# Performance work log

Measured on AMD Instinct MI355X. Metric: run time of the kernel, lower is better.

The kernel has to match this reference:

```python
import jax, jax.numpy as jnp
import numpy as np

N_NODES = 100000
N_EDGES = 1600000
IN_FEATS = 128
OUT_FEATS = 128


def setup_inputs() -> dict:
    key = jax.random.key(0)
    k1, k2, k3, k4, k5 = jax.random.split(key, 5)
    feat = jax.random.normal(k1, (N_NODES, IN_FEATS), dtype=jnp.float32)
    # He (kaiming) uniform-ish init scale for the weights
    bound = np.sqrt(6.0 / IN_FEATS).astype(np.float32)
    weight_u = jax.random.uniform(k2, (IN_FEATS, OUT_FEATS), jnp.float32, -bound, bound)
    weight_v = jax.random.uniform(k3, (IN_FEATS, OUT_FEATS), jnp.float32, -bound, bound)
    bias = jnp.zeros((OUT_FEATS,), dtype=jnp.float32)
    src = jax.random.randint(k4, (N_EDGES,), 0, N_NODES, dtype=jnp.int32)
    dst = jax.random.randint(k5, (N_EDGES,), 0, N_NODES, dtype=jnp.int32)
    return {"feat": feat, "weight_u": weight_u, "weight_v": weight_v,
            "bias": bias, "src": src, "dst": dst}


def reference(feat, weight_u, weight_v, bias, src, dst):
    n = feat.shape[0]
    # in_feats (128) is not > out_feats (128) -> aggregate first, then matmul
    # m_i = sum_{j in N(i)} h_j  (copy_u + sum over edges)
    agg = jax.ops.segment_sum(feat[src], dst, num_segments=n)  # [N, in_feats]
    rst_u = jnp.matmul(agg, weight_u)                          # [N, out_feats]
    rst_v = jnp.matmul(feat, weight_v)                         # [N, out_feats]
    # in-degree normalization, clamped at 1
    deg = jax.ops.segment_sum(jnp.ones_like(dst, dtype=feat.dtype), dst,
                              num_segments=n)
    norm = 1.0 / jnp.maximum(deg, 1.0)                         # [N]
    out = jax.nn.relu(rst_v + norm[:, None] * rst_u + bias)
    return out
```

## Files before the change

### kernel.cpp

```cpp
#include <hip/hip_runtime.h>
#include <hip/hip_bf16.h>
#include <stdint.h>

#define NN 100000
#define NE 1600000
#define NF 128
#define B_BKT 1563
#define NB2 128
#define EPB (NE / NB2)
#define NCNT (B_BKT * NB2)
#define SC2A ((NCNT + 255) / 256)
#define CONV4 (NN * NF / 4)
#define CONV_BLK ((CONV4 + 255) / 256)
#define SETUP_GRID (NB2 + 16 + CONV_BLK)
#define CAP 3072

typedef __attribute__((ext_vector_type(8))) __bf16 bf16x8;
typedef __attribute__((ext_vector_type(4))) float floatx4;
typedef __attribute__((ext_vector_type(4))) unsigned short ushortx4;
typedef __attribute__((ext_vector_type(8))) unsigned short ushortx8;

static __device__ __forceinline__ unsigned short f2bf(float x) {
    union { float f; unsigned u; } v; v.f = x;
    unsigned r = v.u + 0x7fffu + ((v.u >> 16) & 1u);
    return (unsigned short)(r >> 16);
}
static __device__ __forceinline__ float bflo(unsigned w) {
    union { unsigned u; float f; } v; v.u = w << 16; return v.f;
}
static __device__ __forceinline__ float bfhi(unsigned w) {
    union { unsigned u; float f; } v; v.u = w & 0xffff0000u; return v.f;
}

__global__ void k_setup(const float* __restrict__ feat, unsigned short* __restrict__ featb,
                        const float* __restrict__ wv, const float* __restrict__ wu,
                        unsigned short* __restrict__ w2t,
                        const int* __restrict__ dst, int* __restrict__ counts) {
    __shared__ int h[B_BKT];
    int b = blockIdx.x;
    int tid = threadIdx.x;
    if (b < NB2) {
        for (int i = tid; i < B_BKT; i += 256) h[i] = 0;
        __syncthreads();
        int base = b * EPB, end = base + EPB;
        for (int i = base + tid; i < end; i += 256) {
            int d = __builtin_nontemporal_load(&dst[i]);
            atomicAdd(&h[d >> 6], 1);
        }
        __syncthreads();
        for (int i = tid; i < B_BKT; i += 256)
            counts[i * NB2 + b] = h[i];
    } else if (b < NB2 + 16) {
        int id = (b - NB2) * 256 + tid;
        if (id < 128 * 32) {
            int n = id >> 5, kg = id & 31;
            const float* srcm = (kg < 16) ? wv : wu;
            int k0 = (kg & 15) * 8;
            ushortx8 o;
#pragma unroll
            for (int j = 0; j < 8; ++j)
                o[j] = f2bf(srcm[(k0 + j) * 128 + n]);
            int dchunk = n * 32 + (kg ^ (n & 7));
            *(ushortx8*)(w2t + dchunk * 8) = o;
        }
    } else {
        int i = (b - NB2 - 16) * 256 + tid;
        if (i < CONV4) {
            floatx4 f = __builtin_nontemporal_load((const floatx4*)feat + i);
            ushortx4 o;
            o.x = f2bf(f.x); o.y = f2bf(f.y); o.z = f2bf(f.z); o.w = f2bf(f.w);
            __builtin_nontemporal_store(o, (ushortx4*)featb + i);
        }
    }
}

__global__ void k_scan2_a(int* __restrict__ counts, int* __restrict__ bsums) {
    __shared__ int sh[256];
    int i = blockIdx.x * 256 + threadIdx.x;
    int v = (i < NCNT) ? counts[i] : 0;
    sh[threadIdx.x] = v;
    __syncthreads();
    for (int off = 1; off < 256; off <<= 1) {
        int u = (threadIdx.x >= off) ? sh[threadIdx.x - off] : 0;
        __syncthreads();
        sh[threadIdx.x] += u;
        __syncthreads();
    }
    if (i < NCNT) counts[i] = sh[threadIdx.x] - v;
    if (threadIdx.x == 255) bsums[blockIdx.x] = sh[255];
}
__global__ void k_scan2_b(int* __restrict__ bsums) {
    __shared__ int sh[1024];
    int t = threadIdx.x;
    int v = (t < SC2A) ? bsums[t] : 0;
    sh[t] = v;
    __syncthreads();
    for (int off = 1; off < 1024; off <<= 1) {
        int u = (t >= off) ? sh[t - off] : 0;
        __syncthreads();
        sh[t] += u;
        __syncthreads();
    }
    if (t < SC2A) bsums[t] = sh[t] - v;
}

__global__ void k_binscatter(const int* __restrict__ src, const int* __restrict__ dst,
                             const int* __restrict__ counts, const int* __restrict__ bsums,
                             unsigned* __restrict__ streams) {
    __shared__ int cur[B_BKT];
    int tid = threadIdx.x;
    for (int i = tid; i < B_BKT; i += 512) {
        int idx = i * NB2 + blockIdx.x;
        cur[i] = counts[idx] + bsums[idx >> 8];
    }
    __syncthreads();
    int base = blockIdx.x * EPB, end = base + EPB;
    for (int i = base + tid; i < end; i += 512) {
        int d = __builtin_nontemporal_load(&dst[i]);
        int s = __builtin_nontemporal_load(&src[i]);
        int b = d >> 6;
        unsigned packed = ((unsigned)(d & 63) << 17) | (unsigned)s;
        int pos = atomicAdd(&cur[b], 1);
        streams[pos] = packed;
    }
}

__global__ __launch_bounds__(512, 8) void k_agggemm(
    const unsigned* __restrict__ streams,
    const int* __restrict__ counts, const int* __restrict__ bsums,
    const unsigned short* __restrict__ featb,
    const unsigned short* __restrict__ w2t,
    const float* __restrict__ bias,
    float* __restrict__ out) {
    __shared__ int hist[64];
    __shared__ int nodeoff[65];
    __shared__ int eb[CAP];
    __shared__ unsigned short aggt[64 * NF];
    __shared__ int nextn;
    int tid = threadIdx.x;
    int bkt = blockIdx.x;
    int idx = bkt * NB2;
    int s = counts[idx] + bsums[idx >> 8];
    int e = (bkt == B_BKT - 1) ? NE : (counts[idx + NB2] + bsums[(idx + NB2) >> 8]);
    int seg = e - s;
    int lane = tid & 63, wave = tid >> 6;

    if (tid < 64) hist[tid] = 0;
    if (tid == 0) nextn = 0;
    __syncthreads();
    for (int i = s + tid; i < e; i += 512)
        atomicAdd(&hist[streams[i] >> 17], 1);
    __syncthreads();
    if (tid == 0) {
        int run = 0;
#pragma unroll
        for (int n = 0; n < 64; ++n) { nodeoff[n] = run; run += hist[n]; }
        nodeoff[64] = run;
    }
    __syncthreads();
    if (tid < 64) hist[tid] = nodeoff[tid];
    __syncthreads();

    if (seg <= CAP) {
        for (int i = s + tid; i < e; i += 512) {
            unsigned v = streams[i];
            int p = atomicAdd(&hist[v >> 17], 1);
            eb[p] = (int)(v & 0x1FFFFu);
        }
        __syncthreads();
        for (;;) {
            int nl;
            if (lane == 0) nl = atomicAdd(&nextn, 1);
            nl = __shfl(nl, 0, 64);
            if (nl >= 64) break;
            int node = bkt * 64 + nl;
            if (node >= NN) continue;
            int s0 = nodeoff[nl], s1 = nodeoff[nl + 1];
            float a0 = 0.f, a1 = 0.f;
            for (int base = s0; base < s1; base += 64) {
                int ee = (base + lane < s1) ? eb[base + lane] : 0;
                int m = s1 - base; if (m > 64) m = 64;
                int j = 0;
                for (; j + 8 <= m; j += 8) {
                    unsigned w0 = *(const unsigned*)(featb + (size_t)__shfl(ee, j + 0, 64) * NF + lane * 2);
                    unsigned w1 = *(const unsigned*)(featb + (size_t)__shfl(ee, j + 1, 64) * NF + lane * 2);
                    unsigned w2 = *(const unsigned*)(featb + (size_t)__shfl(ee, j + 2, 64) * NF + lane * 2);
                    unsigned w3 = *(const unsigned*)(featb + (size_t)__shfl(ee, j + 3, 64) * NF + lane * 2);
                    unsigned w4 = *(const unsigned*)(featb + (size_t)__shfl(ee, j + 4, 64) * NF + lane * 2);
                    unsigned w5 = *(const unsigned*)(featb + (size_t)__shfl(ee, j + 5, 64) * NF + lane * 2);
                    unsigned w6 = *(const unsigned*)(featb + (size_t)__shfl(ee, j + 6, 64) * NF + lane * 2);
                    unsigned w7 = *(const unsigned*)(featb + (size_t)__shfl(ee, j + 7, 64) * NF + lane * 2);
                    a0 += bflo(w0) + bflo(w1) + bflo(w2) + bflo(w3)
                        + bflo(w4) + bflo(w5) + bflo(w6) + bflo(w7);
                    a1 += bfhi(w0) + bfhi(w1) + bfhi(w2) + bfhi(w3)
                        + bfhi(w4) + bfhi(w5) + bfhi(w6) + bfhi(w7);
                }
                for (; j < m; ++j) {
                    int nn = __shfl(ee, j, 64);
                    unsigned w = *(const unsigned*)(featb + (size_t)nn * NF + lane * 2);
                    a0 += bflo(w); a1 += bfhi(w);
                }
            }
            int dg = s1 - s0; if (dg < 1) dg = 1;
            float scale = 1.0f / (float)dg;
            unsigned outw = ((unsigned)f2bf(a1 * scale) << 16) | (unsigned)f2bf(a0 * scale);
            *(unsigned*)((char*)aggt + nl * 256 + ((lane * 4) ^ ((nl & 7) << 4))) = outw;
        }
    } else {
        for (int nl = wave * 8; nl < wave * 8 + 8; ++nl) {
            int node = bkt * 64 + nl;
            if (node >= NN) break;
            float a0 = 0.f, a1 = 0.f;
            int dg = 0;
            for (int i = s; i < e; ++i) {
                unsigned v = streams[i];
                if ((int)(v >> 17) == nl) {
                    ++dg;
                    unsigned w = *(const unsigned*)(featb + (size_t)(v & 0x1FFFFu) * NF + lane * 2);
                    a0 += bflo(w); a1 += bfhi(w);
                }
            }
            int dc = dg < 1 ? 1 : dg;
            float scale = 1.0f / (float)dc;
            unsigned outw = ((unsigned)f2bf(a1 * scale) << 16) | (unsigned)f2bf(a0 * scale);
            *(unsigned*)((char*)aggt + nl * 256 + ((lane * 4) ^ ((nl & 7) << 4))) = outw;
        }
    }
    __syncthreads();

    int quad = lane >> 4, l15 = lane & 15;
    int rg = wave & 3, ch = wave >> 2;
    int rbl = rg * 16;
    int rb = bkt * 64 + rbl;
    int ar = rb + l15; if (ar > NN - 1) ar = NN - 1;
    const unsigned short* fr = featb + (size_t)ar * NF;
    int lrow = rbl + l15;
    bf16x8 a[8];
#pragma unroll
    for (int ks = 0; ks < 4; ++ks)
        a[ks] = *(const bf16x8*)(fr + ks * 32 + quad * 8);
#pragma unroll
    for (int ks = 0; ks < 4; ++ks) {
        int boff = (ks * 64 + quad * 16) ^ ((lrow & 7) << 4);
        a[4 + ks] = *(const bf16x8*)((const char*)aggt + lrow * 256 + boff);
    }
    float bsv[4];
#pragma unroll
    for (int c = 0; c < 4; ++c) bsv[c] = bias[(ch * 4 + c) * 16 + l15];
#pragma unroll 2
    for (int c = 0; c < 4; ++c) {
        int ct = ch * 4 + c;
        int n = ct * 16 + l15;
        const unsigned short* wrow = w2t + (n << 8);
        int sw = n & 7;
        floatx4 acc = (floatx4){0.f, 0.f, 0.f, 0.f};
#pragma unroll
        for (int ks = 0; ks < 8; ++ks) {
            int kg = ks * 4 + quad;
            bf16x8 b = *(const bf16x8*)(wrow + ((kg ^ sw) << 3));
            acc = __builtin_amdgcn_mfma_f32_16x16x32_bf16(a[ks], b, acc, 0, 0, 0);
        }
#pragma unroll
        for (int r = 0; r < 4; ++r) {
            int row = rb + quad * 4 + r;
            if (row < NN) {
                float v = acc[r] + bsv[c];
                out[(size_t)row * NF + ct * 16 + l15] = v > 0.f ? v : 0.f;
            }
        }
    }
}

extern "C" void kernel_launch(void* const* d_in, const int* in_sizes, int n_in,
                              void* d_out, int out_size, void* d_ws, size_t ws_size,
                              hipStream_t stream) {
    const float* feat = (const float*)d_in[0];
    const float* wu   = (const float*)d_in[1];
    const float* wv   = (const float*)d_in[2];
    const float* bias = (const float*)d_in[3];
    const int* src    = (const int*)d_in[4];
    const int* dst    = (const int*)d_in[5];
    float* out        = (float*)d_out;

    char* ws = (char*)d_ws;
    int* counts           = (int*)(ws + 0);
    int* bsums            = (int*)(ws + 800256);
    unsigned* streams     = (unsigned*)(ws + 1204480);
    unsigned short* featb = (unsigned short*)(ws + 7604480);
    unsigned short* w2t   = (unsigned short*)(ws + 58804480);

    k_setup<<<SETUP_GRID, 256, 0, stream>>>(feat, featb, wv, wu, w2t, dst, counts);
    k_scan2_a<<<SC2A, 256, 0, stream>>>(counts, bsums);
    k_scan2_b<<<1, 1024, 0, stream>>>(bsums);
    k_binscatter<<<NB2, 512, 0, stream>>>(src, dst, counts, bsums, streams);
    k_agggemm<<<B_BKT, 512, 0, stream>>>(streams, counts, bsums, featb, w2t, bias, out);
}
```

Before: 285.8 us.

## Fuse histogram, scan and bin-scatter into one cooperative kernel with grid syncs

Merges the setup, two-level scan and bin-scatter kernels into a single cooperative-launch kernel of 256 blocks that uses grid-wide syncs between the histogram, the per-bucket column scan and the scatter phases. Each bucket's column is scanned by one wave using shuffles, and bucket totals are prefix-summed redundantly inside every block, so the aggregation kernel reads plain offsets. The intent is to remove three kernel launches and their gaps. In exchange, the feat-to-bf16 conversion now runs on only 256 blocks in a grid-stride loop rather than a wide grid, and the scan is done redundantly per block.

After: 369.2 us. +29.2%, slower.

```diff
diff --git a/kernel.cpp b/kernel.cpp
--- a/kernel.cpp
+++ b/kernel.cpp
@@ -1,18 +1,18 @@
 #include <hip/hip_runtime.h>
 #include <hip/hip_bf16.h>
+#include <hip/hip_cooperative_groups.h>
 #include <stdint.h>
+
+namespace cg = cooperative_groups;
 
 #define NN 100000
 #define NE 1600000
 #define NF 128
 #define B_BKT 1563
-#define NB2 128
+#define NB2 256
 #define EPB (NE / NB2)
-#define NCNT (B_BKT * NB2)
-#define SC2A ((NCNT + 255) / 256)
+#define BPB ((B_BKT + NB2 - 1) / NB2)
 #define CONV4 (NN * NF / 4)
-#define CONV_BLK ((CONV4 + 255) / 256)
-#define SETUP_GRID (NB2 + 16 + CONV_BLK)
 #define CAP 3072
 
 typedef __attribute__((ext_vector_type(8))) __bf16 bf16x8;
@@ -32,102 +32,118 @@
     union { unsigned u; float f; } v; v.u = w & 0xffff0000u; return v.f;
 }
 
-__global__ void k_setup(const float* __restrict__ feat, unsigned short* __restrict__ featb,
+__global__ void k_front(const float* __restrict__ feat, unsigned short* __restrict__ featb,
                         const float* __restrict__ wv, const float* __restrict__ wu,
                         unsigned short* __restrict__ w2t,
-                        const int* __restrict__ dst, int* __restrict__ counts) {
-    __shared__ int h[B_BKT];
-    int b = blockIdx.x;
-    int tid = threadIdx.x;
-    if (b < NB2) {
-        for (int i = tid; i < B_BKT; i += 256) h[i] = 0;
+                        const int* __restrict__ src, const int* __restrict__ dst,
+                        int* __restrict__ counts, int* __restrict__ T,
+                        int* __restrict__ offs, unsigned* __restrict__ streams) {
+    __shared__ int sh[B_BKT + 1];
+    __shared__ int part[512];
+    int blk = blockIdx.x, tid = threadIdx.x;
+    int lane = tid & 63, wave = tid >> 6;
+
+    for (int i = tid; i < B_BKT; i += 512) sh[i] = 0;
+    __syncthreads();
+    {
+        int base = blk * EPB, end = base + EPB;
+        for (int i = base + tid; i < end; i += 512)
+            atomicAdd(&sh[__builtin_nontemporal_load(&dst[i]) >> 6], 1);
+    }
+    __syncthreads();
+    for (int i = tid; i < B_BKT; i += 512)
+        counts[i * NB2 + blk] = sh[i];
+    if (blk < 8) {
+        int id = blk * 512 + tid;
+        int n = id >> 5, kg = id & 31;
+        const float* srcm = (kg < 16) ? wv : wu;
+        int k0 = (kg & 15) * 8;
+        ushortx8 o;
+#pragma unroll
+        for (int j = 0; j < 8; ++j)
+            o[j] = f2bf(srcm[(k0 + j) * 128 + n]);
+        *(ushortx8*)(w2t + (n * 32 + (kg ^ (n & 7))) * 8) = o;
+    }
+    for (int i = blk * 512 + tid; i < CONV4; i += NB2 * 512) {
+        floatx4 f = __builtin_nontemporal_load((const floatx4*)feat + i);
+        ushortx4 o;
+        o.x = f2bf(f.x); o.y = f2bf(f.y); o.z = f2bf(f.z); o.w = f2bf(f.w);
+        __builtin_nontemporal_store(o, (ushortx4*)featb + i);
+    }
+    cg::this_grid().sync();
+
+    {
+        int b0 = blk * BPB;
+        for (int bb = wave; bb < BPB; bb += 8) {
+            int b = b0 + bb;
+            if (b < B_BKT) {
+                int* col = counts + b * NB2;
+                int run = 0;
+#pragma unroll
+                for (int sg = 0; sg < 4; ++sg) {
+                    int v = col[sg * 64 + lane];
+                    int x = v;
+#pragma unroll
+                    for (int off = 1; off < 64; off <<= 1) {
+                        int y = __shfl_up(x, off, 64);
+                        if (lane >= off) x += y;
+                    }
+                    col[sg * 64 + lane] = run + x - v;
+                    run += __shfl(x, 63, 64);
+                }
+                if (lane == 0) T[b] = run;
+            }
+        }
+    }
+    cg::this_grid().sync();
+
+    for (int i = tid; i < B_BKT; i += 512) sh[i] = T[i];
+    __syncthreads();
+    {
+        int base4 = tid * 4;
+        int v0 = 0, v1 = 0, v2 = 0, v3 = 0;
+        if (base4 + 0 < B_BKT) v0 = sh[base4 + 0];
+        if (base4 + 1 < B_BKT) v1 = sh[base4 + 1];
+        if (base4 + 2 < B_BKT) v2 = sh[base4 + 2];
+        if (base4 + 3 < B_BKT) v3 = sh[base4 + 3];
+        int tsum = v0 + v1 + v2 + v3;
+        part[tid] = tsum;
         __syncthreads();
-        int base = b * EPB, end = base + EPB;
-        for (int i = base + tid; i < end; i += 256) {
+        for (int off = 1; off < 512; off <<= 1) {
+            int u = (tid >= off) ? part[tid - off] : 0;
+            __syncthreads();
+            part[tid] += u;
+            __syncthreads();
+        }
+        int excl = part[tid] - tsum;
+        if (base4 + 0 < B_BKT) sh[base4 + 0] = excl;
+        if (base4 + 1 < B_BKT) sh[base4 + 1] = excl + v0;
+        if (base4 + 2 < B_BKT) sh[base4 + 2] = excl + v0 + v1;
+        if (base4 + 3 < B_BKT) sh[base4 + 3] = excl + v0 + v1 + v2;
+    }
+    __syncthreads();
+    for (int i = tid; i < B_BKT; i += 512) {
+        int O = sh[i];
+        if (blk == 0) offs[i] = O;
+        sh[i] = O + counts[i * NB2 + blk];
+    }
+    if (blk == 0 && tid == 0) offs[B_BKT] = NE;
+    __syncthreads();
+    {
+        int base = blk * EPB, end = base + EPB;
+        for (int i = base + tid; i < end; i += 512) {
             int d = __builtin_nontemporal_load(&dst[i]);
-            atomicAdd(&h[d >> 6], 1);
-        }
-        __syncthreads();
-        for (int i = tid; i < B_BKT; i += 256)
-            counts[i * NB2 + b] = h[i];
-    } else if (b < NB2 + 16) {
-        int id = (b - NB2) * 256 + tid;
-        if (id < 128 * 32) {
-            int n = id >> 5, kg = id & 31;
-            const float* srcm = (kg < 16) ? wv : wu;
-            int k0 = (kg & 15) * 8;
-            ushortx8 o;
-#pragma unroll
-            for (int j = 0; j < 8; ++j)
-                o[j] = f2bf(srcm[(k0 + j) * 128 + n]);
-            int dchunk = n * 32 + (kg ^ (n & 7));
-            *(ushortx8*)(w2t + dchunk * 8) = o;
-        }
-    } else {
-        int i = (b - NB2 - 16) * 256 + tid;
-        if (i < CONV4) {
-            floatx4 f = __builtin_nontemporal_load((const floatx4*)feat + i);
-            ushortx4 o;
-            o.x = f2bf(f.x); o.y = f2bf(f.y); o.z = f2bf(f.z); o.w = f2bf(f.w);
-            __builtin_nontemporal_store(o, (ushortx4*)featb + i);
-        }
-    }
-}
-
-__global__ void k_scan2_a(int* __restrict__ counts, int* __restrict__ bsums) {
-    __shared__ int sh[256];
-    int i = blockIdx.x * 256 + threadIdx.x;
-    int v = (i < NCNT) ? counts[i] : 0;
-    sh[threadIdx.x] = v;
-    __syncthreads();
-    for (int off = 1; off < 256; off <<= 1) {
-        int u = (threadIdx.x >= off) ? sh[threadIdx.x - off] : 0;
-        __syncthreads();
-        sh[threadIdx.x] += u;
-        __syncthreads();
-    }
-    if (i < NCNT) counts[i] = sh[threadIdx.x] - v;
-    if (threadIdx.x == 255) bsums[blockIdx.x] = sh[255];
-}
-__global__ void k_scan2_b(int* __restrict__ bsums) {
-    __shared__ int sh[1024];
-    int t = threadIdx.x;
-    int v = (t < SC2A) ? bsums[t] : 0;
-    sh[t] = v;
-    __syncthreads();
-    for (int off = 1; off < 1024; off <<= 1) {
-        int u = (t >= off) ? sh[t - off] : 0;
-        __syncthreads();
-        sh[t] += u;
-        __syncthreads();
-    }
-    if (t < SC2A) bsums[t] = sh[t] - v;
-}
-
-__global__ void k_binscatter(const int* __restrict__ src, const int* __restrict__ dst,
-                             const int* __restrict__ counts, const int* __restrict__ bsums,
-                             unsigned* __restrict__ streams) {
-    __shared__ int cur[B_BKT];
-    int tid = threadIdx.x;
-    for (int i = tid; i < B_BKT; i += 512) {
-        int idx = i * NB2 + blockIdx.x;
-        cur[i] = counts[idx] + bsums[idx >> 8];
-    }
-    __syncthreads();
-    int base = blockIdx.x * EPB, end = base + EPB;
-    for (int i = base + tid; i < end; i += 512) {
-        int d = __builtin_nontemporal_load(&dst[i]);
-        int s = __builtin_nontemporal_load(&src[i]);
-        int b = d >> 6;
-        unsigned packed = ((unsigned)(d & 63) << 17) | (unsigned)s;
-        int pos = atomicAdd(&cur[b], 1);
-        streams[pos] = packed;
+            int s = __builtin_nontemporal_load(&src[i]);
+            unsigned packed = ((unsigned)(d & 63) << 17) | (unsigned)s;
+            int pos = atomicAdd(&sh[d >> 6], 1);
+            streams[pos] = packed;
+        }
     }
 }
 
 __global__ __launch_bounds__(512, 8) void k_agggemm(
     const unsigned* __restrict__ streams,
-    const int* __restrict__ counts, const int* __restrict__ bsums,
+    const int* __restrict__ offs,
     const unsigned short* __restrict__ featb,
     const unsigned short* __restrict__ w2t,
     const float* __restrict__ bias,
@@ -139,9 +155,8 @@
     __shared__ int nextn;
     int tid = threadIdx.x;
     int bkt = blockIdx.x;
-    int idx = bkt * NB2;
-    int s = counts[idx] + bsums[idx >> 8];
-    int e = (bkt == B_BKT - 1) ? NE : (counts[idx + NB2] + bsums[(idx + NB2) >> 8]);
+    int s = offs[bkt];
+    int e = offs[bkt + 1];
     int seg = e - s;
     int lane = tid & 63, wave = tid >> 6;
 
@@ -284,14 +299,16 @@
 
     char* ws = (char*)d_ws;
     int* counts           = (int*)(ws + 0);
-    int* bsums            = (int*)(ws + 800256);
-    unsigned* streams     = (unsigned*)(ws + 1204480);
-    unsigned short* featb = (unsigned short*)(ws + 7604480);
-    unsigned short* w2t   = (unsigned short*)(ws + 58804480);
-
-    k_setup<<<SETUP_GRID, 256, 0, stream>>>(feat, featb, wv, wu, w2t, dst, counts);
-    k_scan2_a<<<SC2A, 256, 0, stream>>>(counts, bsums);
-    k_scan2_b<<<1, 1024, 0, stream>>>(bsums);
-    k_binscatter<<<NB2, 512, 0, stream>>>(src, dst, counts, bsums, streams);
-    k_agggemm<<<B_BKT, 512, 0, stream>>>(streams, counts, bsums, featb, w2t, bias, out);
-}
+    int* T                = (int*)(ws + 1600512);
+    int* offs             = (int*)(ws + 1606768);
+    unsigned* streams     = (unsigned*)(ws + 1613024);
+    unsigned short* featb = (unsigned short*)(ws + 8013024);
+    unsigned short* w2t   = (unsigned short*)(ws + 33613024);
+
+    void* fargs[] = { (void*)&feat, (void*)&featb, (void*)&wv, (void*)&wu,
+                      (void*)&w2t, (void*)&src, (void*)&dst,
+                      (void*)&counts, (void*)&T, (void*)&offs, (void*)&streams };
+    hipLaunchCooperativeKernel((void*)k_front, dim3(NB2), dim3(512),
+                               fargs, 0, stream);
+    k_agggemm<<<B_BKT, 512, 0, stream>>>(streams, offs, featb, w2t, bias, out);
+}
```
